# Performance work log

Measured on AMD Instinct MI355X. Metric: run time of the kernel, lower is better.

The kernel has to match this reference:

```python
import jax, jax.numpy as jnp
import numpy as np

N_NODES = 100000
N_EDGES = 800000
D_FEAT = 64
N_HIDDEN = 64
N_CLASSES = 16


def setup_inputs() -> dict:
    key = jax.random.key(0)
    ks = jax.random.split(key, 10)
    s = 1.0 / np.sqrt(N_HIDDEN)
    inp = {
        "x": jax.random.normal(ks[0], (N_NODES, D_FEAT), dtype=jnp.float32),
        "edge_index": jax.random.randint(ks[1], (2, N_EDGES), 0, N_NODES, dtype=jnp.int64)
        if jax.config.jax_enable_x64 else jax.random.randint(ks[1], (2, N_EDGES), 0, N_NODES, dtype=jnp.int32),
        "W1": jax.random.normal(ks[2], (D_FEAT, N_HIDDEN), dtype=jnp.float32) * s,
        "b1": jnp.zeros((N_HIDDEN,), jnp.float32),
        "W2": jax.random.normal(ks[3], (N_HIDDEN, N_HIDDEN), dtype=jnp.float32) * s,
        "b2": jnp.zeros((N_HIDDEN,), jnp.float32),
        "W3": jax.random.normal(ks[4], (N_HIDDEN, N_HIDDEN), dtype=jnp.float32) * s,
        "b3": jnp.zeros((N_HIDDEN,), jnp.float32),
        "Wf1": jax.random.normal(ks[5], (N_HIDDEN, N_HIDDEN), dtype=jnp.float32) * s,
        "bf1": jnp.zeros((N_HIDDEN,), jnp.float32),
        "Wf2": jax.random.normal(ks[6], (N_HIDDEN, N_HIDDEN), dtype=jnp.float32) * s,
        "bf2": jnp.zeros((N_HIDDEN,), jnp.float32),
        "Wf3": jax.random.normal(ks[7], (N_HIDDEN, N_CLASSES), dtype=jnp.float32) * s,
        "bf3": jnp.zeros((N_CLASSES,), jnp.float32),
    }
    return inp


def reference(x, edge_index, W1, b1, W2, b2, W3, b3, Wf1, bf1, Wf2, bf2, Wf3, bf3):
    N = x.shape[0]
    loops = jnp.arange(N, dtype=edge_index.dtype)
    src = jnp.concatenate([edge_index[0], loops])  # [E+N]
    dst = jnp.concatenate([edge_index[1], loops])
    # symmetric GCN normalization with self-loops (edge weight 1)
    deg = jax.ops.segment_sum(jnp.ones(src.shape[0], x.dtype), dst, num_segments=N)
    dis = jax.lax.rsqrt(jnp.maximum(deg, 1.0))  # deg >= 1 due to self-loops
    norm = dis[src] * dis[dst]  # [E+N]

    def gcn(h, W, b):
        h = h @ W  # [N, H]
        msg = h[src] * norm[:, None]  # [E+N, H] gather
        return jax.ops.segment_sum(msg, dst, num_segments=N) + b  # scatter-add

    y = jax.nn.relu(gcn(x, W1, b1))
    y = jax.nn.relu(gcn(y, W2, b2))
    y = jax.nn.relu(gcn(y, W3, b3))
    y = jax.nn.relu(y @ Wf1 + bf1)
    y = jax.nn.relu(y @ Wf2 + bf2)
    y = y @ Wf3 + bf3
    return jax.nn.log_softmax(y, axis=1)
```

## Files before the change

### kernel.cpp

```cpp
#include <hip/hip_runtime.h>
#include <hip/hip_bf16.h>

#define NN 100000
#define NE 800000
#define EBLK 391
#define NBUK 196
#define BSTRIDE 6144

typedef __attribute__((ext_vector_type(8))) short bf16x8;
typedef __attribute__((ext_vector_type(4))) float f32x4;

__device__ __forceinline__ unsigned short f2b(float f) {
  unsigned int x = __float_as_uint(f);
  return (unsigned short)((x + 0x7fffu + ((x >> 16) & 1u)) >> 16);
}
__device__ __forceinline__ float b2f(short us) {
  return __uint_as_float(((unsigned int)(unsigned short)us) << 16);
}
__device__ __forceinline__ void acc8(float* acc, bf16x8 v) {
#pragma unroll
  for (int i = 0; i < 8; ++i) acc[i] += b2f(v[i]);
}

static __global__ __launch_bounds__(256) void k_scwc(const int* __restrict__ src, const int* __restrict__ dst,
                                                     int* __restrict__ gcur, int* __restrict__ ebuf,
    const float* __restrict__ W1, const float* __restrict__ W2, const float* __restrict__ W3,
    const float* __restrict__ Wf1, const float* __restrict__ Wf2, const float* __restrict__ Wf3,
    short* __restrict__ W1t, short* __restrict__ W2t, short* __restrict__ W3t,
    short* __restrict__ Wf1t, short* __restrict__ Wf2t, short* __restrict__ Wf3t) {
  int tid = threadIdx.x, blk = blockIdx.x;
  if (blk >= EBLK) {
    int b = blk - EBLK;
    if (b < 5) {
      const float* W = (b == 0) ? W1 : (b == 1) ? W2 : (b == 2) ? W3 : (b == 3) ? Wf1 : Wf2;
      short* Wt = (b == 0) ? W1t : (b == 1) ? W2t : (b == 2) ? W3t : (b == 3) ? Wf1t : Wf2t;
#pragma unroll
      for (int i = 0; i < 16; ++i) {
        int idx = tid + 256 * i;
        int k = idx >> 6, nn = idx & 63;
        Wt[nn * 64 + k] = (short)f2b(W[idx]);
      }
    } else {
#pragma unroll
      for (int i = 0; i < 4; ++i) {
        int idx = tid + 256 * i;
        int k = idx >> 4, nn = idx & 15;
        Wf3t[nn * 64 + k] = (short)f2b(Wf3[idx]);
      }
    }
    return;
  }
  __shared__ int hist[256];
  __shared__ int lstart[256];
  __shared__ int gbase[256];
  __shared__ int cur[NBUK];
  __shared__ int2 sbuf[2048];
  hist[tid] = 0;
  __syncthreads();
  int base = blk * 2048;
  int dd[8], ss[8];
#pragma unroll
  for (int i = 0; i < 8; ++i) {
    int e = base + tid + 256 * i;
    if (e < NE) {
      dd[i] = dst[e]; ss[i] = src[e];
      atomicAdd(&hist[dd[i] >> 9], 1);
    } else dd[i] = -1;
  }
  __syncthreads();
  int v = hist[tid];
  lstart[tid] = v;
  __syncthreads();
  for (int off = 1; off < 256; off <<= 1) {
    int t = (tid >= off) ? lstart[tid - off] : 0;
    __syncthreads();
    lstart[tid] += t;
    __syncthreads();
  }
  int excl = lstart[tid] - v;
  __syncthreads();
  lstart[tid] = excl;
  if (tid < NBUK) {
    cur[tid] = 0;
    gbase[tid] = (v > 0) ? atomicAdd(&gcur[tid], v) : 0;
  }
  __syncthreads();
#pragma unroll
  for (int i = 0; i < 8; ++i) {
    if (dd[i] >= 0) {
      int b = dd[i] >> 9;
      int p = atomicAdd(&cur[b], 1);
      sbuf[lstart[b] + p] = make_int2((ss[i] << 9) | (dd[i] & 511), b);
    }
  }
  __syncthreads();
  int m = NE - base; if (m > 2048) m = 2048;
#pragma unroll
  for (int i = 0; i < 8; ++i) {
    int j = tid + 256 * i;
    if (j < m) {
      int2 e = sbuf[j];
      int b = e.y;
      int gpos = b * BSTRIDE + gbase[b] + (j - lstart[b]);
      ebuf[gpos] = e.x;
    }
  }
}

static __global__ __launch_bounds__(256) void k_bucket(const int* __restrict__ ebuf, const int* __restrict__ gcur,
                                                       int4* __restrict__ rc4, float* __restrict__ dis,
                                                       int* __restrict__ col_idx) {
  __shared__ int cnt[512];
  __shared__ int lrs[512];
  __shared__ int sd[256];
  int b = blockIdx.x, tid = threadIdx.x;
  int base_n = b << 9;
  int ebeg = b * BSTRIDE;
  int m = gcur[b];
  cnt[tid] = 0; cnt[tid + 256] = 0;
  __syncthreads();
  for (int j = tid; j < m; j += 256) atomicAdd(&cnt[ebuf[ebeg + j] & 511], 1);
  __syncthreads();
  int v0 = cnt[2 * tid], v1 = cnt[2 * tid + 1];
  int s = v0 + v1;
  sd[tid] = s;
  __syncthreads();
  for (int off = 1; off < 256; off <<= 1) {
    int t = (tid >= off) ? sd[tid - off] : 0;
    __syncthreads();
    sd[tid] += t;
    __syncthreads();
  }
  int excl = sd[tid] - s;
  lrs[2 * tid] = excl;
  lrs[2 * tid + 1] = excl + v0;
  __syncthreads();
  for (int i = tid; i < 512; i += 256) {
    int n = base_n + i;
    if (n < NN) {
      int c = cnt[i];
      float d = 1.0f / sqrtf((float)c + 1.0f);
      rc4[n] = make_int4(ebeg + lrs[i], c, __float_as_int(d), 0);
      dis[n] = d;
    }
  }
  for (int i = tid; i < 512; i += 256) cnt[i] = lrs[i];
  __syncthreads();
  for (int j = tid; j < m; j += 256) {
    int e = ebuf[ebeg + j];
    int p = atomicAdd(&cnt[e & 511], 1);
    col_idx[ebeg + p] = e >> 9;
  }
}

__device__ __forceinline__ bf16x8 load_a_frag_f32(const float* __restrict__ p, bool valid) {
  float4 f0 = valid ? *(const float4*)p : make_float4(0.f, 0.f, 0.f, 0.f);
  float4 f1 = valid ? *(const float4*)(p + 4) : make_float4(0.f, 0.f, 0.f, 0.f);
  bf16x8 a;
  a[0] = (short)f2b(f0.x); a[1] = (short)f2b(f0.y); a[2] = (short)f2b(f0.z); a[3] = (short)f2b(f0.w);
  a[4] = (short)f2b(f1.x); a[5] = (short)f2b(f1.y); a[6] = (short)f2b(f1.z); a[7] = (short)f2b(f1.w);
  return a;
}

__device__ __forceinline__ void mm_body(bf16x8 a0, bf16x8 a1, const short* __restrict__ Wt,
                                        const float* __restrict__ dis, short* __restrict__ out,
                                        int row0, int rlane, int g, int n) {
  f32x4 acc[4];
#pragma unroll
  for (int t = 0; t < 4; ++t) acc[t] = (f32x4){0.f, 0.f, 0.f, 0.f};
#pragma unroll
  for (int t = 0; t < 4; ++t) {
    bf16x8 b0 = *(const bf16x8*)(Wt + (rlane + 16 * t) * 64 + g * 8);
    bf16x8 b1 = *(const bf16x8*)(Wt + (rlane + 16 * t) * 64 + g * 8 + 32);
    acc[t] = __builtin_amdgcn_mfma_f32_16x16x32_bf16(a0, b0, acc[t], 0, 0, 0);
    acc[t] = __builtin_amdgcn_mfma_f32_16x16x32_bf16(a1, b1, acc[t], 0, 0, 0);
  }
#pragma unroll
  for (int r = 0; r < 4; ++r) {
    int gr = row0 + g * 4 + r;
    if (gr < n) {
      float s = dis[gr];
#pragma unroll
      for (int t = 0; t < 4; ++t)
        out[(size_t)gr * 64 + rlane + 16 * t] = (short)f2b(acc[t][r] * s);
    }
  }
}

static __global__ __launch_bounds__(256) void k_mm1(const float* __restrict__ in, const short* __restrict__ Wt,
                                                    const float* __restrict__ dis, short* __restrict__ out, int n) {
  int tid = threadIdx.x;
  int lane = tid & 63, w = tid >> 6;
  int row0 = blockIdx.x * 64 + w * 16;
  int rlane = lane & 15, g = lane >> 4;
  int arow = row0 + rlane;
  bool av = arow < n;
  const float* ap = in + (size_t)arow * 64 + g * 8;
  bf16x8 a0 = load_a_frag_f32(ap, av);
  bf16x8 a1 = load_a_frag_f32(ap + 32, av);
  mm_body(a0, a1, Wt, dis, out, row0, rlane, g, n);
}

__device__ __forceinline__ void agg8_to_lds(const short* __restrict__ ht, const int4* __restrict__ rc4,
                                            const int* __restrict__ col_idx,
                                            const float* __restrict__ bias, short (*Hs)[72],
                                            int nodebase, int wrow0, int lane, int n) {
  int g = lane >> 3, f = lane & 7;
  float4 b0v = *(const float4*)&bias[f * 8];
  float4 b1v = *(const float4*)&bias[f * 8 + 4];
  float bb[8] = {b0v.x, b0v.y, b0v.z, b0v.w, b1v.x, b1v.y, b1v.z, b1v.w};
  int node = nodebase + g;
  bool nv = node < n;
  int4 rcv = nv ? rc4[node] : make_int4(0, 0, 0, 0);
  int beg = rcv.x, cnt = rcv.y;
  float ds = nv ? __int_as_float(rcv.z) : 0.f;
  float acc[8] = {0.f, 0.f, 0.f, 0.f, 0.f, 0.f, 0.f, 0.f};
  if (nv) acc8(acc, *(const bf16x8*)(ht + (size_t)node * 64 + f * 8));
  for (int base = 0; base < cnt; base += 8) {
    int idx = (base + f < cnt) ? col_idx[beg + base + f] : 0;
    int s[8];
#pragma unroll
    for (int e = 0; e < 8; ++e) s[e] = __shfl(idx, g * 8 + e);
    bf16x8 r[8];
#pragma unroll
    for (int e = 0; e < 8; ++e) r[e] = *(const bf16x8*)(ht + (size_t)s[e] * 64 + f * 8);
    int mm = cnt - base; if (mm > 8) mm = 8;
#pragma unroll
    for (int e = 0; e < 8; ++e) { if (e < mm) acc8(acc, r[e]); }
  }
  bf16x8 o;
#pragma unroll
  for (int i = 0; i < 8; ++i)
    o[i] = (short)f2b(fmaxf(fmaf(ds, acc[i], bb[i]), 0.f));
  *(bf16x8*)&Hs[wrow0 + g][f * 8] = o;
}

static __global__ __launch_bounds__(128) void k_aggmm(const short* __restrict__ ht, const int4* __restrict__ rc4,
                                                      const int* __restrict__ col_idx, const float* __restrict__ dis,
                                                      const float* __restrict__ bias, const short* __restrict__ Wt,
                                                      short* __restrict__ out, int n) {
  __shared__ __align__(16) short Hs[16][72];
  int tid = threadIdx.x;
  int lane = tid & 63, w = tid >> 6;
  int row0 = blockIdx.x * 16;
  agg8_to_lds(ht, rc4, col_idx, bias, Hs, row0 + w * 8, w * 8, lane, n);
  __syncthreads();
  int rlane = lane & 15, g = lane >> 4;
  bf16x8 a0 = *(const bf16x8*)&Hs[rlane][g * 8];
  bf16x8 a1 = *(const bf16x8*)&Hs[rlane][g * 8 + 32];
#pragma unroll
  for (int tt = 0; tt < 2; ++tt) {
    int t = 2 * w + tt;
    bf16x8 b0 = *(const bf16x8*)(Wt + (rlane + 16 * t) * 64 + g * 8);
    bf16x8 b1 = *(const bf16x8*)(Wt + (rlane + 16 * t) * 64 + g * 8 + 32);
    f32x4 acc = (f32x4){0.f, 0.f, 0.f, 0.f};
    acc = __builtin_amdgcn_mfma_f32_16x16x32_bf16(a0, b0, acc, 0, 0, 0);
    acc = __builtin_amdgcn_mfma_f32_16x16x32_bf16(a1, b1, acc, 0, 0, 0);
#pragma unroll
    for (int r = 0; r < 4; ++r) {
      int gr = row0 + g * 4 + r;
      if (gr < n) out[(size_t)gr * 64 + rlane + 16 * t] = (short)f2b(acc[r] * dis[gr]);
    }
  }
}

static __global__ __launch_bounds__(128) void k_aggdense(const short* __restrict__ ht, const int4* __restrict__ rc4,
    const int* __restrict__ col_idx, const float* __restrict__ bias,
    const short* __restrict__ W1t, const float* __restrict__ bf1,
    const short* __restrict__ W2t, const float* __restrict__ bf2,
    const short* __restrict__ W3t, const float* __restrict__ bf3,
    float* __restrict__ out, int n) {
  __shared__ __align__(16) short Hs[16][72];
  __shared__ __align__(16) short H2[16][72];
  int tid = threadIdx.x;
  int lane = tid & 63, w = tid >> 6;
  int row0 = blockIdx.x * 16;
  agg8_to_lds(ht, rc4, col_idx, bias, Hs, row0 + w * 8, w * 8, lane, n);
  __syncthreads();
  int rlane = lane & 15, g = lane >> 4;
  {
    bf16x8 a0 = *(const bf16x8*)&Hs[rlane][g * 8];
    bf16x8 a1 = *(const bf16x8*)&Hs[rlane][g * 8 + 32];
#pragma unroll
    for (int tt = 0; tt < 2; ++tt) {
      int t = 2 * w + tt;
      bf16x8 b0 = *(const bf16x8*)(W1t + (rlane + 16 * t) * 64 + g * 8);
      bf16x8 b1 = *(const bf16x8*)(W1t + (rlane + 16 * t) * 64 + g * 8 + 32);
      f32x4 acc = (f32x4){0.f, 0.f, 0.f, 0.f};
      acc = __builtin_amdgcn_mfma_f32_16x16x32_bf16(a0, b0, acc, 0, 0, 0);
      acc = __builtin_amdgcn_mfma_f32_16x16x32_bf16(a1, b1, acc, 0, 0, 0);
      float bb = bf1[16 * t + rlane];
#pragma unroll
      for (int r = 0; r < 4; ++r)
        H2[g * 4 + r][16 * t + rlane] = (short)f2b(fmaxf(acc[r] + bb, 0.f));
    }
  }
  __syncthreads();
  {
    bf16x8 c0 = *(const bf16x8*)&H2[rlane][g * 8];
    bf16x8 c1 = *(const bf16x8*)&H2[rlane][g * 8 + 32];
#pragma unroll
    for (int tt = 0; tt < 2; ++tt) {
      int t = 2 * w + tt;
      bf16x8 b0 = *(const bf16x8*)(W2t + (rlane + 16 * t) * 64 + g * 8);
      bf16x8 b1 = *(const bf16x8*)(W2t + (rlane + 16 * t) * 64 + g * 8 + 32);
      f32x4 acc = (f32x4){0.f, 0.f, 0.f, 0.f};
      acc = __builtin_amdgcn_mfma_f32_16x16x32_bf16(c0, b0, acc, 0, 0, 0);
      acc = __builtin_amdgcn_mfma_f32_16x16x32_bf16(c1, b1, acc, 0, 0, 0);
      float bb = bf2[16 * t + rlane];
#pragma unroll
      for (int r = 0; r < 4; ++r)
        Hs[g * 4 + r][16 * t + rlane] = (short)f2b(fmaxf(acc[r] + bb, 0.f));
    }
  }
  __syncthreads();
  if (w == 0) {
    bf16x8 d0 = *(const bf16x8*)&Hs[rlane][g * 8];
    bf16x8 d1 = *(const bf16x8*)&Hs[rlane][g * 8 + 32];
    bf16x8 e0 = *(const bf16x8*)(W3t + rlane * 64 + g * 8);
    bf16x8 e1 = *(const bf16x8*)(W3t + rlane * 64 + g * 8 + 32);
    f32x4 z = (f32x4){0.f, 0.f, 0.f, 0.f};
    z = __builtin_amdgcn_mfma_f32_16x16x32_bf16(d0, e0, z, 0, 0, 0);
    z = __builtin_amdgcn_mfma_f32_16x16x32_bf16(d1, e1, z, 0, 0, 0);
    float bsc = bf3[rlane];
#pragma unroll
    for (int r = 0; r < 4; ++r) {
      float zz = z[r] + bsc;
      float mx = zz;
      mx = fmaxf(mx, __shfl_xor(mx, 1));
      mx = fmaxf(mx, __shfl_xor(mx, 2));
      mx = fmaxf(mx, __shfl_xor(mx, 4));
      mx = fmaxf(mx, __shfl_xor(mx, 8));
      float ex = __expf(zz - mx);
      ex += __shfl_xor(ex, 1);
      ex += __shfl_xor(ex, 2);
      ex += __shfl_xor(ex, 4);
      ex += __shfl_xor(ex, 8);
      float lse = mx + __logf(ex);
      int gr = row0 + g * 4 + r;
      if (gr < n) out[(size_t)gr * 16 + rlane] = zz - lse;
    }
  }
}

extern "C" void kernel_launch(void* const* d_in, const int* in_sizes, int n_in,
                              void* d_out, int out_size, void* d_ws, size_t ws_size,
                              hipStream_t stream) {
  (void)in_sizes; (void)n_in; (void)out_size; (void)ws_size;
  const float* x   = (const float*)d_in[0];
  const int*   ei  = (const int*)d_in[1];
  const float* W1  = (const float*)d_in[2];
  const float* b1  = (const float*)d_in[3];
  const float* W2  = (const float*)d_in[4];
  const float* b2  = (const float*)d_in[5];
  const float* W3  = (const float*)d_in[6];
  const float* b3  = (const float*)d_in[7];
  const float* Wf1 = (const float*)d_in[8];
  const float* bf1 = (const float*)d_in[9];
  const float* Wf2 = (const float*)d_in[10];
  const float* bf2 = (const float*)d_in[11];
  const float* Wf3 = (const float*)d_in[12];
  const float* bf3 = (const float*)d_in[13];
  float* outp = (float*)d_out;
  const int* srcp = ei;
  const int* dstp = ei + NE;

  char* ws = (char*)d_ws;
  size_t off = 0;
  auto alloc = [&](size_t bytes) { void* p = ws + off; off = (off + bytes + 255) & ~(size_t)255; return p; };
  int4*  rc4    = (int4*)alloc((size_t)NN * 16);
  float* dis    = (float*)alloc((size_t)NN * 4);
  int*   gcur   = (int*)alloc(256 * 4);
  int*   colidx = (int*)alloc((size_t)NBUK * BSTRIDE * 4);
  short* W1t    = (short*)alloc(4096 * 2);
  short* W2t    = (short*)alloc(4096 * 2);
  short* W3t    = (short*)alloc(4096 * 2);
  short* Wf1t   = (short*)alloc(4096 * 2);
  short* Wf2t   = (short*)alloc(4096 * 2);
  short* Wf3t   = (short*)alloc(1024 * 2);
  short* bufA   = (short*)alloc((size_t)NN * 64 * 2);
  short* bufB   = (short*)alloc((size_t)NN * 64 * 2);
  int*   ebuf   = (int*)alloc((size_t)NBUK * BSTRIDE * 4);

  int gMM = (NN + 63) / 64;
  int gAG = (NN + 15) / 16;

  hipMemsetAsync(gcur, 0, 256 * 4, stream);
  k_scwc<<<EBLK + 6, 256, 0, stream>>>(srcp, dstp, gcur, ebuf,
                                       W1, W2, W3, Wf1, Wf2, Wf3,
                                       W1t, W2t, W3t, Wf1t, Wf2t, Wf3t);
  k_bucket<<<NBUK, 256, 0, stream>>>(ebuf, gcur, rc4, dis, colidx);

  k_mm1<<<gMM, 256, 0, stream>>>(x, W1t, dis, bufB, NN);
  k_aggmm<<<gAG, 128, 0, stream>>>(bufB, rc4, colidx, dis, b1, W2t, bufA, NN);
  k_aggmm<<<gAG, 128, 0, stream>>>(bufA, rc4, colidx, dis, b2, W3t, bufB, NN);
  k_aggdense<<<gAG, 128, 0, stream>>>(bufB, rc4, colidx, b3,
                                      Wf1t, bf1, Wf2t, bf2, Wf3t, bf3, outp, NN);
}
```

Measured before the change: 135.0 us.

## Quantize intermediate node features to int8 with per-row scales for gathers

Transformed node features are now stored as int8 with one float scale per row (the max-abs value times the degree normalization), replacing bf16 storage. The gather-heavy aggregation reads 8 bytes per lane instead of 16, plus a per-edge scale lookup, which halves feature gather traffic. In exchange it adds a cross-lane max reduction in the matmul epilogues, an extra scale gather per edge, and noticeably lower precision in the intermediate activations, which may push outputs past the tolerance.

```diff
diff --git a/kernel.cpp b/kernel.cpp
--- a/kernel.cpp
+++ b/kernel.cpp
@@ -14,12 +14,16 @@
   unsigned int x = __float_as_uint(f);
   return (unsigned short)((x + 0x7fffu + ((x >> 16) & 1u)) >> 16);
 }
-__device__ __forceinline__ float b2f(short us) {
-  return __uint_as_float(((unsigned int)(unsigned short)us) << 16);
-}
-__device__ __forceinline__ void acc8(float* acc, bf16x8 v) {
-#pragma unroll
-  for (int i = 0; i < 8; ++i) acc[i] += b2f(v[i]);
+__device__ __forceinline__ void accq(float* acc, uint2 v, float s) {
+  int lo = (int)v.x, hi = (int)v.y;
+  acc[0] += s * (float)((lo << 24) >> 24);
+  acc[1] += s * (float)((lo << 16) >> 24);
+  acc[2] += s * (float)((lo << 8)  >> 24);
+  acc[3] += s * (float)( lo        >> 24);
+  acc[4] += s * (float)((hi << 24) >> 24);
+  acc[5] += s * (float)((hi << 16) >> 24);
+  acc[6] += s * (float)((hi << 8)  >> 24);
+  acc[7] += s * (float)( hi        >> 24);
 }
 
 static __global__ __launch_bounds__(256) void k_scwc(const int* __restrict__ src, const int* __restrict__ dst,
@@ -162,9 +166,10 @@
   return a;
 }
 
-__device__ __forceinline__ void mm_body(bf16x8 a0, bf16x8 a1, const short* __restrict__ Wt,
-                                        const float* __restrict__ dis, short* __restrict__ out,
-                                        int row0, int rlane, int g, int n) {
+__device__ __forceinline__ void mm_body_q(bf16x8 a0, bf16x8 a1, const short* __restrict__ Wt,
+                                          const float* __restrict__ dis, char* __restrict__ out,
+                                          float* __restrict__ hscale,
+                                          int row0, int rlane, int g, int n) {
   f32x4 acc[4];
 #pragma unroll
   for (int t = 0; t < 4; ++t) acc[t] = (f32x4){0.f, 0.f, 0.f, 0.f};
@@ -177,18 +182,27 @@
   }
 #pragma unroll
   for (int r = 0; r < 4; ++r) {
+    float m = 0.f;
+#pragma unroll
+    for (int t = 0; t < 4; ++t) m = fmaxf(m, fabsf(acc[t][r]));
+    m = fmaxf(m, __shfl_xor(m, 1));
+    m = fmaxf(m, __shfl_xor(m, 2));
+    m = fmaxf(m, __shfl_xor(m, 4));
+    m = fmaxf(m, __shfl_xor(m, 8));
     int gr = row0 + g * 4 + r;
     if (gr < n) {
-      float s = dis[gr];
+      float inv = (m > 0.f) ? 127.f / m : 0.f;
+      if (rlane == 0) hscale[gr] = dis[gr] * m * (1.f / 127.f);
 #pragma unroll
       for (int t = 0; t < 4; ++t)
-        out[(size_t)gr * 64 + rlane + 16 * t] = (short)f2b(acc[t][r] * s);
+        out[(size_t)gr * 64 + rlane + 16 * t] = (char)(int)rintf(acc[t][r] * inv);
     }
   }
 }
 
 static __global__ __launch_bounds__(256) void k_mm1(const float* __restrict__ in, const short* __restrict__ Wt,
-                                                    const float* __restrict__ dis, short* __restrict__ out, int n) {
+                                                    const float* __restrict__ dis, char* __restrict__ out,
+                                                    float* __restrict__ hscale, int n) {
   int tid = threadIdx.x;
   int lane = tid & 63, w = tid >> 6;
   int row0 = blockIdx.x * 64 + w * 16;
@@ -198,13 +212,13 @@
   const float* ap = in + (size_t)arow * 64 + g * 8;
   bf16x8 a0 = load_a_frag_f32(ap, av);
   bf16x8 a1 = load_a_frag_f32(ap + 32, av);
-  mm_body(a0, a1, Wt, dis, out, row0, rlane, g, n);
-}
-
-__device__ __forceinline__ void agg8_to_lds(const short* __restrict__ ht, const int4* __restrict__ rc4,
-                                            const int* __restrict__ col_idx,
-                                            const float* __restrict__ bias, short (*Hs)[72],
-                                            int nodebase, int wrow0, int lane, int n) {
+  mm_body_q(a0, a1, Wt, dis, out, hscale, row0, rlane, g, n);
+}
+
+__device__ __forceinline__ void agg8q_to_lds(const char* __restrict__ ht, const float* __restrict__ hscale,
+                                             const int4* __restrict__ rc4, const int* __restrict__ col_idx,
+                                             const float* __restrict__ bias, short (*Hs)[72],
+                                             int nodebase, int wrow0, int lane, int n) {
   int g = lane >> 3, f = lane & 7;
   float4 b0v = *(const float4*)&bias[f * 8];
   float4 b1v = *(const float4*)&bias[f * 8 + 4];
@@ -215,18 +229,23 @@
   int beg = rcv.x, cnt = rcv.y;
   float ds = nv ? __int_as_float(rcv.z) : 0.f;
   float acc[8] = {0.f, 0.f, 0.f, 0.f, 0.f, 0.f, 0.f, 0.f};
-  if (nv) acc8(acc, *(const bf16x8*)(ht + (size_t)node * 64 + f * 8));
+  if (nv) accq(acc, *(const uint2*)(ht + (size_t)node * 64 + f * 8), hscale[node]);
   for (int base = 0; base < cnt; base += 8) {
-    int idx = (base + f < cnt) ? col_idx[beg + base + f] : 0;
-    int s[8];
-#pragma unroll
-    for (int e = 0; e < 8; ++e) s[e] = __shfl(idx, g * 8 + e);
-    bf16x8 r[8];
-#pragma unroll
-    for (int e = 0; e < 8; ++e) r[e] = *(const bf16x8*)(ht + (size_t)s[e] * 64 + f * 8);
+    int eidx = base + f;
+    int idx = (eidx < cnt) ? col_idx[beg + eidx] : 0;
+    float sc = (eidx < cnt) ? hscale[idx] : 0.f;
+    int s[8]; float ss[8];
+#pragma unroll
+    for (int e = 0; e < 8; ++e) {
+      s[e] = __shfl(idx, g * 8 + e);
+      ss[e] = __shfl(sc, g * 8 + e);
+    }
+    uint2 r[8];
+#pragma unroll
+    for (int e = 0; e < 8; ++e) r[e] = *(const uint2*)(ht + (size_t)s[e] * 64 + f * 8);
     int mm = cnt - base; if (mm > 8) mm = 8;
 #pragma unroll
-    for (int e = 0; e < 8; ++e) { if (e < mm) acc8(acc, r[e]); }
+    for (int e = 0; e < 8; ++e) { if (e < mm) accq(acc, r[e], ss[e]); }
   }
   bf16x8 o;
 #pragma unroll
@@ -235,37 +254,25 @@
   *(bf16x8*)&Hs[wrow0 + g][f * 8] = o;
 }
 
-static __global__ __launch_bounds__(128) void k_aggmm(const short* __restrict__ ht, const int4* __restrict__ rc4,
-                                                      const int* __restrict__ col_idx, const float* __restrict__ dis,
-                                                      const float* __restrict__ bias, const short* __restrict__ Wt,
-                                                      short* __restrict__ out, int n) {
+static __global__ __launch_bounds__(128) void k_aggmm(const char* __restrict__ ht, const float* __restrict__ hscale,
+                                                      const int4* __restrict__ rc4, const int* __restrict__ col_idx,
+                                                      const float* __restrict__ dis, const float* __restrict__ bias,
+                                                      const short* __restrict__ Wt,
+                                                      char* __restrict__ out, float* __restrict__ oscale, int n) {
   __shared__ __align__(16) short Hs[16][72];
   int tid = threadIdx.x;
   int lane = tid & 63, w = tid >> 6;
   int row0 = blockIdx.x * 16;
-  agg8_to_lds(ht, rc4, col_idx, bias, Hs, row0 + w * 8, w * 8, lane, n);
+  agg8q_to_lds(ht, hscale, rc4, col_idx, bias, Hs, row0 + w * 8, w * 8, lane, n);
   __syncthreads();
   int rlane = lane & 15, g = lane >> 4;
   bf16x8 a0 = *(const bf16x8*)&Hs[rlane][g * 8];
   bf16x8 a1 = *(const bf16x8*)&Hs[rlane][g * 8 + 32];
-#pragma unroll
-  for (int tt = 0; tt < 2; ++tt) {
-    int t = 2 * w + tt;
-    bf16x8 b0 = *(const bf16x8*)(Wt + (rlane + 16 * t) * 64 + g * 8);
-    bf16x8 b1 = *(const bf16x8*)(Wt + (rlane + 16 * t) * 64 + g * 8 + 32);
-    f32x4 acc = (f32x4){0.f, 0.f, 0.f, 0.f};
-    acc = __builtin_amdgcn_mfma_f32_16x16x32_bf16(a0, b0, acc, 0, 0, 0);
-    acc = __builtin_amdgcn_mfma_f32_16x16x32_bf16(a1, b1, acc, 0, 0, 0);
-#pragma unroll
-    for (int r = 0; r < 4; ++r) {
-      int gr = row0 + g * 4 + r;
-      if (gr < n) out[(size_t)gr * 64 + rlane + 16 * t] = (short)f2b(acc[r] * dis[gr]);
-    }
-  }
-}
-
-static __global__ __launch_bounds__(128) void k_aggdense(const short* __restrict__ ht, const int4* __restrict__ rc4,
-    const int* __restrict__ col_idx, const float* __restrict__ bias,
+  mm_body_q(a0, a1, Wt, dis, out, oscale, row0, rlane, g, n);
+}
+
+static __global__ __launch_bounds__(128) void k_aggdense(const char* __restrict__ ht, const float* __restrict__ hscale,
+    const int4* __restrict__ rc4, const int* __restrict__ col_idx, const float* __restrict__ bias,
     const short* __restrict__ W1t, const float* __restrict__ bf1,
     const short* __restrict__ W2t, const float* __restrict__ bf2,
     const short* __restrict__ W3t, const float* __restrict__ bf3,
@@ -275,7 +282,7 @@
   int tid = threadIdx.x;
   int lane = tid & 63, w = tid >> 6;
   int row0 = blockIdx.x * 16;
-  agg8_to_lds(ht, rc4, col_idx, bias, Hs, row0 + w * 8, w * 8, lane, n);
+  agg8q_to_lds(ht, hscale, rc4, col_idx, bias, Hs, row0 + w * 8, w * 8, lane, n);
   __syncthreads();
   int rlane = lane & 15, g = lane >> 4;
   {
@@ -378,8 +385,10 @@
   short* Wf1t   = (short*)alloc(4096 * 2);
   short* Wf2t   = (short*)alloc(4096 * 2);
   short* Wf3t   = (short*)alloc(1024 * 2);
-  short* bufA   = (short*)alloc((size_t)NN * 64 * 2);
-  short* bufB   = (short*)alloc((size_t)NN * 64 * 2);
+  char*  htA    = (char*)alloc((size_t)NN * 64);
+  float* scA    = (float*)alloc((size_t)NN * 4);
+  char*  htB    = (char*)alloc((size_t)NN * 64);
+  float* scB    = (float*)alloc((size_t)NN * 4);
   int*   ebuf   = (int*)alloc((size_t)NBUK * BSTRIDE * 4);
 
   int gMM = (NN + 63) / 64;
@@ -391,9 +400,9 @@
                                        W1t, W2t, W3t, Wf1t, Wf2t, Wf3t);
   k_bucket<<<NBUK, 256, 0, stream>>>(ebuf, gcur, rc4, dis, colidx);
 
-  k_mm1<<<gMM, 256, 0, stream>>>(x, W1t, dis, bufB, NN);
-  k_aggmm<<<gAG, 128, 0, stream>>>(bufB, rc4, colidx, dis, b1, W2t, bufA, NN);
-  k_aggmm<<<gAG, 128, 0, stream>>>(bufA, rc4, colidx, dis, b2, W3t, bufB, NN);
-  k_aggdense<<<gAG, 128, 0, stream>>>(bufB, rc4, colidx, b3,
+  k_mm1<<<gMM, 256, 0, stream>>>(x, W1t, dis, htB, scB, NN);
+  k_aggmm<<<gAG, 128, 0, stream>>>(htB, scB, rc4, colidx, dis, b1, W2t, htA, scA, NN);
+  k_aggmm<<<gAG, 128, 0, stream>>>(htA, scA, rc4, colidx, dis, b2, W3t, htB, scB, NN);
+  k_aggdense<<<gAG, 128, 0, stream>>>(htB, scB, rc4, colidx, b3,
                                       Wf1t, bf1, Wf2t, bf2, Wf3t, bf3, outp, NN);
 }
```

After: 149.7 us. 10.8% more time.

## Use wave-level shuffle scans and single-wave aggregation blocks without barriers

Applied to the files above, without the earlier changes.

The shared-memory Hillis-Steele scans in the edge bucketing kernels become wavefront shuffle scans combined through a small per-wave sum array, which cuts many block barriers. The aggregation+MFMA kernels now use one 64-thread wave per block handling 8 rows, so all __syncthreads are dropped. Each wave computes all four output column tiles, but half the MFMA rows are padding. Smaller blocks double the block count and waste half of the MFMA work in exchange for no inter-wave synchronisation.

```diff
diff --git a/kernel.cpp b/kernel.cpp
--- a/kernel.cpp
+++ b/kernel.cpp
@@ -54,7 +54,9 @@
   __shared__ int lstart[256];
   __shared__ int gbase[256];
   __shared__ int cur[NBUK];
+  __shared__ int wsum[4];
   __shared__ int2 sbuf[2048];
+  int lane = tid & 63, wv = tid >> 6;
   hist[tid] = 0;
   __syncthreads();
   int base = blk * 2048;
@@ -69,16 +71,18 @@
   }
   __syncthreads();
   int v = hist[tid];
-  lstart[tid] = v;
-  __syncthreads();
-  for (int off = 1; off < 256; off <<= 1) {
-    int t = (tid >= off) ? lstart[tid - off] : 0;
-    __syncthreads();
-    lstart[tid] += t;
-    __syncthreads();
-  }
-  int excl = lstart[tid] - v;
-  __syncthreads();
+  int s = v;
+#pragma unroll
+  for (int off = 1; off < 64; off <<= 1) {
+    int t = __shfl_up(s, off);
+    if (lane >= off) s += t;
+  }
+  if (lane == 63) wsum[wv] = s;
+  __syncthreads();
+  int wpre = 0;
+#pragma unroll
+  for (int i = 0; i < 4; ++i) wpre += (i < wv) ? wsum[i] : 0;
+  int excl = s + wpre - v;
   lstart[tid] = excl;
   if (tid < NBUK) {
     cur[tid] = 0;
@@ -112,8 +116,9 @@
                                                        int* __restrict__ col_idx) {
   __shared__ int cnt[512];
   __shared__ int lrs[512];
-  __shared__ int sd[256];
+  __shared__ int wsum[4];
   int b = blockIdx.x, tid = threadIdx.x;
+  int lane = tid & 63, wv = tid >> 6;
   int base_n = b << 9;
   int ebeg = b * BSTRIDE;
   int m = gcur[b];
@@ -122,16 +127,19 @@
   for (int j = tid; j < m; j += 256) atomicAdd(&cnt[ebuf[ebeg + j] & 511], 1);
   __syncthreads();
   int v0 = cnt[2 * tid], v1 = cnt[2 * tid + 1];
-  int s = v0 + v1;
-  sd[tid] = s;
-  __syncthreads();
-  for (int off = 1; off < 256; off <<= 1) {
-    int t = (tid >= off) ? sd[tid - off] : 0;
-    __syncthreads();
-    sd[tid] += t;
-    __syncthreads();
-  }
-  int excl = sd[tid] - s;
+  int sv = v0 + v1;
+  int s = sv;
+#pragma unroll
+  for (int off = 1; off < 64; off <<= 1) {
+    int t = __shfl_up(s, off);
+    if (lane >= off) s += t;
+  }
+  if (lane == 63) wsum[wv] = s;
+  __syncthreads();
+  int wpre = 0;
+#pragma unroll
+  for (int i = 0; i < 4; ++i) wpre += (i < wv) ? wsum[i] : 0;
+  int excl = s + wpre - sv;
   lrs[2 * tid] = excl;
   lrs[2 * tid + 1] = excl + v0;
   __syncthreads();
@@ -235,36 +243,42 @@
   *(bf16x8*)&Hs[wrow0 + g][f * 8] = o;
 }
 
-static __global__ __launch_bounds__(128) void k_aggmm(const short* __restrict__ ht, const int4* __restrict__ rc4,
-                                                      const int* __restrict__ col_idx, const float* __restrict__ dis,
-                                                      const float* __restrict__ bias, const short* __restrict__ Wt,
-                                                      short* __restrict__ out, int n) {
+static __global__ __launch_bounds__(64) void k_aggmm(const short* __restrict__ ht, const int4* __restrict__ rc4,
+                                                     const int* __restrict__ col_idx, const float* __restrict__ dis,
+                                                     const float* __restrict__ bias, const short* __restrict__ Wt,
+                                                     short* __restrict__ out, int n) {
   __shared__ __align__(16) short Hs[16][72];
-  int tid = threadIdx.x;
-  int lane = tid & 63, w = tid >> 6;
-  int row0 = blockIdx.x * 16;
-  agg8_to_lds(ht, rc4, col_idx, bias, Hs, row0 + w * 8, w * 8, lane, n);
-  __syncthreads();
+  int lane = threadIdx.x;
+  int row0 = blockIdx.x * 8;
+  agg8_to_lds(ht, rc4, col_idx, bias, Hs, row0, 0, lane, n);
   int rlane = lane & 15, g = lane >> 4;
   bf16x8 a0 = *(const bf16x8*)&Hs[rlane][g * 8];
   bf16x8 a1 = *(const bf16x8*)&Hs[rlane][g * 8 + 32];
-#pragma unroll
-  for (int tt = 0; tt < 2; ++tt) {
-    int t = 2 * w + tt;
+  f32x4 acc[4];
+#pragma unroll
+  for (int t = 0; t < 4; ++t) acc[t] = (f32x4){0.f, 0.f, 0.f, 0.f};
+#pragma unroll
+  for (int t = 0; t < 4; ++t) {
     bf16x8 b0 = *(const bf16x8*)(Wt + (rlane + 16 * t) * 64 + g * 8);
     bf16x8 b1 = *(const bf16x8*)(Wt + (rlane + 16 * t) * 64 + g * 8 + 32);
-    f32x4 acc = (f32x4){0.f, 0.f, 0.f, 0.f};
-    acc = __builtin_amdgcn_mfma_f32_16x16x32_bf16(a0, b0, acc, 0, 0, 0);
-    acc = __builtin_amdgcn_mfma_f32_16x16x32_bf16(a1, b1, acc, 0, 0, 0);
+    acc[t] = __builtin_amdgcn_mfma_f32_16x16x32_bf16(a0, b0, acc[t], 0, 0, 0);
+    acc[t] = __builtin_amdgcn_mfma_f32_16x16x32_bf16(a1, b1, acc[t], 0, 0, 0);
+  }
+  if (g < 2) {
 #pragma unroll
     for (int r = 0; r < 4; ++r) {
       int gr = row0 + g * 4 + r;
-      if (gr < n) out[(size_t)gr * 64 + rlane + 16 * t] = (short)f2b(acc[r] * dis[gr]);
-    }
-  }
-}
-
-static __global__ __launch_bounds__(128) void k_aggdense(const short* __restrict__ ht, const int4* __restrict__ rc4,
+      if (gr < n) {
+        float s = dis[gr];
+#pragma unroll
+        for (int t = 0; t < 4; ++t)
+          out[(size_t)gr * 64 + rlane + 16 * t] = (short)f2b(acc[t][r] * s);
+      }
+    }
+  }
+}
+
+static __global__ __launch_bounds__(64) void k_aggdense(const short* __restrict__ ht, const int4* __restrict__ rc4,
     const int* __restrict__ col_idx, const float* __restrict__ bias,
     const short* __restrict__ W1t, const float* __restrict__ bf1,
     const short* __restrict__ W2t, const float* __restrict__ bf2,
@@ -272,49 +286,47 @@
     float* __restrict__ out, int n) {
   __shared__ __align__(16) short Hs[16][72];
   __shared__ __align__(16) short H2[16][72];
-  int tid = threadIdx.x;
-  int lane = tid & 63, w = tid >> 6;
-  int row0 = blockIdx.x * 16;
-  agg8_to_lds(ht, rc4, col_idx, bias, Hs, row0 + w * 8, w * 8, lane, n);
-  __syncthreads();
+  int lane = threadIdx.x;
+  int row0 = blockIdx.x * 8;
+  agg8_to_lds(ht, rc4, col_idx, bias, Hs, row0, 0, lane, n);
   int rlane = lane & 15, g = lane >> 4;
   {
     bf16x8 a0 = *(const bf16x8*)&Hs[rlane][g * 8];
     bf16x8 a1 = *(const bf16x8*)&Hs[rlane][g * 8 + 32];
 #pragma unroll
-    for (int tt = 0; tt < 2; ++tt) {
-      int t = 2 * w + tt;
+    for (int t = 0; t < 4; ++t) {
       bf16x8 b0 = *(const bf16x8*)(W1t + (rlane + 16 * t) * 64 + g * 8);
       bf16x8 b1 = *(const bf16x8*)(W1t + (rlane + 16 * t) * 64 + g * 8 + 32);
       f32x4 acc = (f32x4){0.f, 0.f, 0.f, 0.f};
       acc = __builtin_amdgcn_mfma_f32_16x16x32_bf16(a0, b0, acc, 0, 0, 0);
       acc = __builtin_amdgcn_mfma_f32_16x16x32_bf16(a1, b1, acc, 0, 0, 0);
-      float bb = bf1[16 * t + rlane];
-#pragma unroll
-      for (int r = 0; r < 4; ++r)
-        H2[g * 4 + r][16 * t + rlane] = (short)f2b(fmaxf(acc[r] + bb, 0.f));
-    }
-  }
-  __syncthreads();
+      if (g < 2) {
+        float bb = bf1[16 * t + rlane];
+#pragma unroll
+        for (int r = 0; r < 4; ++r)
+          H2[g * 4 + r][16 * t + rlane] = (short)f2b(fmaxf(acc[r] + bb, 0.f));
+      }
+    }
+  }
   {
     bf16x8 c0 = *(const bf16x8*)&H2[rlane][g * 8];
     bf16x8 c1 = *(const bf16x8*)&H2[rlane][g * 8 + 32];
 #pragma unroll
-    for (int tt = 0; tt < 2; ++tt) {
-      int t = 2 * w + tt;
+    for (int t = 0; t < 4; ++t) {
       bf16x8 b0 = *(const bf16x8*)(W2t + (rlane + 16 * t) * 64 + g * 8);
       bf16x8 b1 = *(const bf16x8*)(W2t + (rlane + 16 * t) * 64 + g * 8 + 32);
       f32x4 acc = (f32x4){0.f, 0.f, 0.f, 0.f};
       acc = __builtin_amdgcn_mfma_f32_16x16x32_bf16(c0, b0, acc, 0, 0, 0);
       acc = __builtin_amdgcn_mfma_f32_16x16x32_bf16(c1, b1, acc, 0, 0, 0);
-      float bb = bf2[16 * t + rlane];
-#pragma unroll
-      for (int r = 0; r < 4; ++r)
-        Hs[g * 4 + r][16 * t + rlane] = (short)f2b(fmaxf(acc[r] + bb, 0.f));
-    }
-  }
-  __syncthreads();
-  if (w == 0) {
+      if (g < 2) {
+        float bb = bf2[16 * t + rlane];
+#pragma unroll
+        for (int r = 0; r < 4; ++r)
+          Hs[g * 4 + r][16 * t + rlane] = (short)f2b(fmaxf(acc[r] + bb, 0.f));
+      }
+    }
+  }
+  {
     bf16x8 d0 = *(const bf16x8*)&Hs[rlane][g * 8];
     bf16x8 d1 = *(const bf16x8*)&Hs[rlane][g * 8 + 32];
     bf16x8 e0 = *(const bf16x8*)(W3t + rlane * 64 + g * 8);
@@ -338,7 +350,7 @@
       ex += __shfl_xor(ex, 8);
       float lse = mx + __logf(ex);
       int gr = row0 + g * 4 + r;
-      if (gr < n) out[(size_t)gr * 16 + rlane] = zz - lse;
+      if (g < 2 && gr < n) out[(size_t)gr * 16 + rlane] = zz - lse;
     }
   }
 }
@@ -383,7 +395,7 @@
   int*   ebuf   = (int*)alloc((size_t)NBUK * BSTRIDE * 4);
 
   int gMM = (NN + 63) / 64;
-  int gAG = (NN + 15) / 16;
+  int gAG = (NN + 7) / 8;
 
   hipMemsetAsync(gcur, 0, 256 * 4, stream);
   k_scwc<<<EBLK + 6, 256, 0, stream>>>(srcp, dstp, gcur, ebuf,
@@ -392,8 +404,8 @@
   k_bucket<<<NBUK, 256, 0, stream>>>(ebuf, gcur, rc4, dis, colidx);
 
   k_mm1<<<gMM, 256, 0, stream>>>(x, W1t, dis, bufB, NN);
-  k_aggmm<<<gAG, 128, 0, stream>>>(bufB, rc4, colidx, dis, b1, W2t, bufA, NN);
-  k_aggmm<<<gAG, 128, 0, stream>>>(bufA, rc4, colidx, dis, b2, W3t, bufB, NN);
-  k_aggdense<<<gAG, 128, 0, stream>>>(bufB, rc4, colidx, b3,
-                                      Wf1t, bf1, Wf2t, bf2, Wf3t, bf3, outp, NN);
-}
+  k_aggmm<<<gAG, 64, 0, stream>>>(bufB, rc4, colidx, dis, b1, W2t, bufA, NN);
+  k_aggmm<<<gAG, 64, 0, stream>>>(bufA, rc4, colidx, dis, b2, W3t, bufB, NN);
+  k_aggdense<<<gAG, 64, 0, stream>>>(bufB, rc4, colidx, b3,
+                                     Wf1t, bf1, Wf2t, bf2, Wf3t, bf3, outp, NN);
+}
```

Result: slower. 158.6 us (+17.4%).
